# Kernel tuning notes

Measured on AMD Instinct MI355X. Metric: run time of the kernel, lower is better.

## Reference

```python
import jax, jax.numpy as jnp
import numpy as np

N_QUBITS = 12
N_LAYERS = 3


def _apply_ry(state, theta, q):
    # state: (2,)*n real statevector; RY on qubit q
    c = jnp.cos(theta * 0.5)
    s = jnp.sin(theta * 0.5)
    st = jnp.moveaxis(state, q, 0)
    st = jnp.stack([c * st[0] - s * st[1], s * st[0] + c * st[1]])
    return jnp.moveaxis(st, 0, q)


def _apply_cz(state, q, r):
    st = jnp.moveaxis(state, (q, r), (0, 1))
    st = st.at[1, 1].multiply(-1.0)
    return jnp.moveaxis(st, (0, 1), (q, r))


def _embed(x, params):
    # angle-embedding ansatz: L layers of RY(theta[l,q]+x[q]) + CZ ring
    n = N_QUBITS
    state = jnp.zeros((2,) * n, dtype=x.dtype).at[(0,) * n].set(1.0)
    for l in range(N_LAYERS):
        for q in range(n):
            state = _apply_ry(state, params[l, q] + x[q], q)
        for q in range(n):
            state = _apply_cz(state, q, (q + 1) % n)
    return state.reshape(-1)  # (2^n,)


def setup_inputs() -> dict:
    key = jax.random.key(0)
    k1, k2, k3 = jax.random.split(key, 3)
    data = jax.random.uniform(k1, (2048, N_QUBITS), dtype=jnp.float32)
    labels = jax.random.randint(k2, (2048,), 0, 2, dtype=jnp.int32)
    params = jax.random.normal(k3, (N_LAYERS, N_QUBITS), dtype=jnp.float32)
    return {"data": data, "labels": labels, "params": params}


def reference(data, labels, params):
    # Psi[i] = U(x_i, params)|0>, k_ij = |<psi_j|psi_i>|^2 (== prob of amp 0 of U^dag(x_j)U(x_i)|0>)
    psi = jax.vmap(_embed, in_axes=(0, None))(data, params)  # (N, 2^n)
    K = jnp.square(psi @ psi.T)                              # (N, N) pairwise kernel
    lab = 2.0 * labels.astype(psi.dtype) - 1.0               # {0,1} -> {-1,+1}
    LL = jnp.outer(lab, lab)
    kernel_polarity = jnp.sum(LL * K)
    square_sum_k = jnp.sum(K * K)
    square_sum_l = jnp.sum(LL * LL)
    return kernel_polarity / jnp.sqrt(square_sum_k * square_sum_l)
```

## Files before the change

kernel.cpp:

```cpp
#include <hip/hip_runtime.h>
#include <math.h>

#define NQ    12
#define DIM   4096
#define K_EXT 4096
#define KSL   512
#define NSAMP 2048
#define NLAY  3
#define NT2   16
#define NTRI2 136
#define NSLICE 8
#define BK    64

typedef __attribute__((ext_vector_type(8)))  short bf16x8;
typedef __attribute__((ext_vector_type(16))) float floatx16;

__device__ __forceinline__ unsigned short f32_to_bf16(float x) {
    unsigned u = __builtin_bit_cast(unsigned, x);
    u += 0x7FFFu + ((u >> 16) & 1u);
    return (unsigned short)(u >> 16);
}

__device__ __forceinline__ void gl_lds16(const unsigned short* g, unsigned short* l) {
    __builtin_amdgcn_global_load_lds(
        (const __attribute__((address_space(1))) unsigned int*)g,
        (__attribute__((address_space(3))) unsigned int*)l,
        16, 0, 0);
}

__device__ __forceinline__ void tri_decode(int bid, int& bi, int& bj) {
    int i = (int)((33.0 - sqrt(33.0*33.0 - 8.0*(double)bid)) * 0.5);
    int start = i*(33-i)/2;
    while (bid < start)               { --i; start = i*(33-i)/2; }
    while (bid >= start + (NT2 - i))  { start += NT2 - i; ++i; }
    bi = i; bj = i + (bid - start);
}

__global__ __launch_bounds__(256) void sim_kernel(const float* __restrict__ data,
                                                  const float* __restrict__ params,
                                                  unsigned short* __restrict__ pe,
                                                  double* __restrict__ acc,
                                                  unsigned* __restrict__ cnt)
{
    __shared__ float CS[2*36], SN[2*36];
    __shared__ float trans[2][4608];
    const int tid  = threadIdx.x;
    const int wave = tid >> 6, lane = tid & 63;
    const int sidx = wave >> 1;
    const int w    = wave & 1;
    const int smp  = blockIdx.x * 2 + sidx;

    if (blockIdx.x == 0 && tid == 0) {
        acc[0] = 0.0; acc[1] = 0.0; cnt[0] = 0u;
    }

    if (w == 0 && lane < NLAY*NQ) {
        const int q = lane % NQ;
        const float th = 0.5f * (params[lane] + data[smp*NQ + q]);
        CS[sidx*36 + lane] = cosf(th);
        SN[sidx*36 + lane] = sinf(th);
    }
    __syncthreads();

    float v[32];

    float* buf = trans[sidx];
    float* wb  = buf + 36*lane + 2304*w;
    const float* rb = buf + ((lane>>2)&15) + 16*w + 36*(lane&3);

    {
        const float* cs = &CS[sidx*36];
        const float* sn = &SN[sidx*36];
        const int hi = (lane >> 2) & 15;
        float fx = ((lane & 1) ? sn[0] : cs[0]) * ((lane & 2) ? sn[1] : cs[1]);
        fx *= ((hi & 1) ? sn[7]  : cs[7]);
        fx *= ((hi & 2) ? sn[8]  : cs[8]);
        fx *= ((hi & 4) ? sn[9]  : cs[9]);
        fx *= ((hi & 8) ? sn[10] : cs[10]);
        fx *= (w ? sn[11] : cs[11]);
        v[0] = fx * cs[2];
        v[1] = fx * sn[2];
        #pragma unroll
        for (int b = 1; b < 5; ++b) {
            const int M = 1 << b;
            #pragma unroll
            for (int r = 0; r < 32; ++r) {
                if (r < M) {
                    v[r | M] = v[r] * sn[2 + b];
                    v[r]     = v[r] * cs[2 + b];
                }
            }
        }
        const int Base = (lane & 3) | (hi << 7) | (w << 11);
        #pragma unroll
        for (int r = 0; r < 32; ++r) {
            const int i  = Base | (r << 2);
            const int t  = ((i >> 1) | (i << 11)) & 0xFFF;
            const int p  = __popc(i & t) & 1;
            v[r] = __builtin_bit_cast(float, __builtin_bit_cast(int, v[r]) ^ (p << 31));
        }
    }

    #pragma unroll 1
    for (int l = 1; l < NLAY; ++l) {
        const float* cs = &CS[sidx*36 + l*NQ];
        const float* sn = &SN[sidx*36 + l*NQ];
        const int even = !(l & 1);

        {
            const int qb = even ? 7 : 2;
            #pragma unroll
            for (int b = 0; b < 5; ++b) {
                const float c = cs[qb + b], s = sn[qb + b];
                const int M = 1 << b;
                #pragma unroll
                for (int r = 0; r < 32; ++r) {
                    if (!(r & M)) {
                        const float a0 = v[r], a1 = v[r | M];
                        v[r]     = c * a0 - s * a1;
                        v[r | M] = s * a0 + c * a1;
                    }
                }
            }
        }
        {
            const float c0 = cs[0], s0 = sn[0];
            const float t0 = (lane & 1) ? s0 : -s0;
            #pragma unroll
            for (int r = 0; r < 32; ++r) {
                const int iv = __builtin_bit_cast(int, v[r]);
                const int pv = __builtin_amdgcn_update_dpp(0, iv, 0xB1, 0xF, 0xF, true);
                v[r] = c0 * v[r] + t0 * __builtin_bit_cast(float, pv);
            }
            const float c1 = cs[1], s1 = sn[1];
            const float t1 = (lane & 2) ? s1 : -s1;
            #pragma unroll
            for (int r = 0; r < 32; ++r) {
                const int iv = __builtin_bit_cast(int, v[r]);
                const int pv = __builtin_amdgcn_update_dpp(0, iv, 0x4E, 0xF, 0xF, true);
                v[r] = c1 * v[r] + t1 * __builtin_bit_cast(float, pv);
            }
        }
        __syncthreads();
        #pragma unroll
        for (int t = 0; t < 8; ++t) {
            float4 q4;
            q4.x = v[4*t]; q4.y = v[4*t+1]; q4.z = v[4*t+2]; q4.w = v[4*t+3];
            *(float4*)&wb[4*t] = q4;
        }
        __syncthreads();
        #pragma unroll
        for (int r = 0; r < 32; ++r)
            v[r] = rb[144*(r & 15) + 2304*(r >> 4)];

        {
            const int qb = even ? 2 : 7;
            #pragma unroll
            for (int b = 0; b < 5; ++b) {
                const float c = cs[qb + b], s = sn[qb + b];
                const int M = 1 << b;
                #pragma unroll
                for (int r = 0; r < 32; ++r) {
                    if (!(r & M)) {
                        const float a0 = v[r], a1 = v[r | M];
                        v[r]     = c * a0 - s * a1;
                        v[r | M] = s * a0 + c * a1;
                    }
                }
            }
        }
        {
            const int Base = even ? ((lane & 3) | (((lane >> 2) & 15) << 7) | (w << 11))
                                  : (lane | (w << 6));
            const int shift = even ? 2 : 7;
            #pragma unroll
            for (int r = 0; r < 32; ++r) {
                const int i  = Base | (r << shift);
                const int t  = ((i >> 1) | (i << 11)) & 0xFFF;
                const int p  = __popc(i & t) & 1;
                v[r] = __builtin_bit_cast(float, __builtin_bit_cast(int, v[r]) ^ (p << 31));
            }
        }
    }

    const int sw = smp & 7;
    const int ell = w*64 + lane;
    unsigned short* outb = pe + (size_t)smp * K_EXT;
    #pragma unroll
    for (int c = 0; c < 4; ++c) {
        uint4 H;
        H.x = (unsigned)f32_to_bf16(v[c*8+0]) | ((unsigned)f32_to_bf16(v[c*8+1]) << 16);
        H.y = (unsigned)f32_to_bf16(v[c*8+2]) | ((unsigned)f32_to_bf16(v[c*8+3]) << 16);
        H.z = (unsigned)f32_to_bf16(v[c*8+4]) | ((unsigned)f32_to_bf16(v[c*8+5]) << 16);
        H.w = (unsigned)f32_to_bf16(v[c*8+6]) | ((unsigned)f32_to_bf16(v[c*8+7]) << 16);
        const int gc  = 4*ell + c;
        const int pos = (gc & ~7) | ((gc ^ sw) & 7);
        *(uint4*)&outb[pos*8] = H;
    }
}

__global__ __launch_bounds__(256) void gram_partial(const unsigned short* __restrict__ pe,
                                                    float* __restrict__ Gp)
{
    __shared__ __align__(16) unsigned short stage[2][2*128*64];

    const int tid   = threadIdx.x;
    const int tile  = blockIdx.x >> 3;
    const int slice = blockIdx.x & 7;
    int bi, bj; tri_decode(tile, bi, bj);
    const int k0 = slice * KSL;

    const int wave = tid >> 6, lane = tid & 63;
    const int qr = (wave >> 1) * 64;
    const int qc = (wave &  1) * 64;
    const int mrow = lane & 31;
    const int chsel = lane >> 5;
    const int sw = mrow & 7;

    floatx16 c00, c01, c10, c11;
    #pragma unroll
    for (int i = 0; i < 16; ++i) { c00[i]=0.f; c01[i]=0.f; c10[i]=0.f; c11[i]=0.f; }

    const int mat  = wave >> 1;
    const int half = wave & 1;
    const unsigned short* gbase = pe
        + ((size_t)((mat ? bj : bi)*128 + half*64 + (lane >> 3))) * K_EXT
        + k0 + (lane & 7)*8;
    const int lofs = mat*128*64 + half*64*64;

    {
        unsigned short* l = &stage[0][lofs];
        #pragma unroll
        for (int i = 0; i < 8; ++i)
            gl_lds16(gbase + (size_t)i*8*K_EXT, l + i*512);
    }
    __syncthreads();

    int cur = 0;
    #pragma unroll 1
    for (int kk = 0; kk < KSL; kk += BK) {
        if (kk + BK < KSL) {
            unsigned short* l = &stage[cur ^ 1][lofs];
            const unsigned short* g = gbase + kk + BK;
            #pragma unroll
            for (int i = 0; i < 8; ++i)
                gl_lds16(g + (size_t)i*8*K_EXT, l + i*512);
        }

        const unsigned short* As = &stage[cur][0];
        const unsigned short* Bs = &stage[cur][128*64];
        #pragma unroll
        for (int ks = 0; ks < 4; ++ks) {
            const int ch = (ks*2 + chsel) ^ sw;
            const bf16x8 a0 = *(const bf16x8*)&As[(qr +      mrow)*64 + ch*8];
            const bf16x8 a1 = *(const bf16x8*)&As[(qr + 32 + mrow)*64 + ch*8];
            const bf16x8 b0 = *(const bf16x8*)&Bs[(qc +      mrow)*64 + ch*8];
            const bf16x8 b1 = *(const bf16x8*)&Bs[(qc + 32 + mrow)*64 + ch*8];
            c00 = __builtin_amdgcn_mfma_f32_32x32x16_bf16(a0, b0, c00, 0, 0, 0);
            c01 = __builtin_amdgcn_mfma_f32_32x32x16_bf16(a0, b1, c01, 0, 0, 0);
            c10 = __builtin_amdgcn_mfma_f32_32x32x16_bf16(a1, b0, c10, 0, 0, 0);
            c11 = __builtin_amdgcn_mfma_f32_32x32x16_bf16(a1, b1, c11, 0, 0, 0);
        }
        __syncthreads();
        cur ^= 1;
    }

    float* Gt = Gp + ((size_t)slice * NTRI2 + tile) * 16384;
    const int crow = chsel * 4;
    const int ccol = lane & 31;
    #pragma unroll
    for (int rr = 0; rr < 16; ++rr) {
        const int rl = (rr & 3) + 8*(rr >> 2) + crow;
        const int r0 = qr + rl,  r1 = qr + 32 + rl;
        const int cA = qc + ccol, cB = qc + 32 + ccol;
        Gt[r0*128 + cA] = c00[rr];
        Gt[r0*128 + cB] = c01[rr];
        Gt[r1*128 + cA] = c10[rr];
        Gt[r1*128 + cB] = c11[rr];
    }
}

__global__ __launch_bounds__(256) void gram_reduce(const float* __restrict__ Gp,
                                                   const int* __restrict__ labels,
                                                   double* __restrict__ acc,
                                                   unsigned* __restrict__ cnt,
                                                   float* __restrict__ out)
{
    __shared__ float la[128], lb[128];
    __shared__ double red1[256], red2[256];
    const int tid  = threadIdx.x;
    const int tile = blockIdx.x >> 2;
    const int quar = blockIdx.x & 3;
    int bi, bj; tri_decode(tile, bi, bj);

    if (tid < 128) la[tid]       = 2.0f*(float)labels[bi*128 + tid]       - 1.0f;
    else           lb[tid - 128] = 2.0f*(float)labels[bj*128 + tid - 128] - 1.0f;
    __syncthreads();

    const size_t stride = (size_t)NTRI2 * 16384;
    const float* g0 = Gp + (size_t)tile * 16384 + quar * 4096;

    double s1 = 0.0, s2 = 0.0;
    #pragma unroll
    for (int u = 0; u < 4; ++u) {
        const int e = u*1024 + tid*4;
        float4 g = make_float4(0.f, 0.f, 0.f, 0.f);
        #pragma unroll
        for (int s = 0; s < NSLICE; ++s) {
            const float4 t = *(const float4*)&g0[e + (size_t)s*stride];
            g.x += t.x; g.y += t.y; g.z += t.z; g.w += t.w;
        }
        const int ge  = quar*4096 + e;
        const int row = ge >> 7, c0 = ge & 127;
        const float lr = la[row];
        const float gg[4] = {g.x, g.y, g.z, g.w};
        #pragma unroll
        for (int j = 0; j < 4; ++j) {
            const int col = c0 + j;
            const float w = (bi < bj) ? 2.0f : ((row < col) ? 2.0f : ((row == col) ? 1.0f : 0.0f));
            const float g2 = gg[j] * gg[j];
            s1 += (double)(w * lr * lb[col] * g2);
            const double d = (double)g2;
            s2 += (double)w * d * d;
        }
    }

    red1[tid] = s1; red2[tid] = s2; __syncthreads();
    for (int off = 128; off; off >>= 1) {
        if (tid < off) { red1[tid] += red1[tid+off]; red2[tid] += red2[tid+off]; }
        __syncthreads();
    }
    if (tid == 0) {
        atomicAdd(&acc[0], red1[0]);
        atomicAdd(&acc[1], red2[0]);
        __threadfence();
        const unsigned old = atomicAdd(cnt, 1u);
        if (old == NTRI2*4 - 1) {
            const double t1 = atomicAdd(&acc[0], 0.0);
            const double t2 = atomicAdd(&acc[1], 0.0);
            out[0] = (float)(t1 / (sqrt(t2) * (double)NSAMP));
        }
    }
}

extern "C" void kernel_launch(void* const* d_in, const int* in_sizes, int n_in,
                              void* d_out, int out_size, void* d_ws, size_t ws_size,
                              hipStream_t stream)
{
    const float* data   = (const float*)d_in[0];
    const int*   labels = (const int*)d_in[1];
    const float* params = (const float*)d_in[2];

    double*   acc = (double*)d_ws;
    unsigned* cnt = (unsigned*)((char*)d_ws + 64);
    unsigned short* psi = (unsigned short*)((char*)d_ws + 16384);
    float* Gp = (float*)((char*)d_ws + 16384 + (size_t)NSAMP*K_EXT*2);

    sim_kernel<<<NSAMP/2, 256, 0, stream>>>(data, params, psi, acc, cnt);
    gram_partial<<<NTRI2*NSLICE, 256, 0, stream>>>(psi, Gp);
    gram_reduce<<<NTRI2*4, 256, 0, stream>>>(Gp, labels, acc, cnt, (float*)d_out);
}
```

Measured before the change: 138.3 us.

## Fuse gram reduction into split-K kernel via per-tile completion counters

Removes the separate reduce kernel: each gram_partial block bumps a per-tile counter, and the last slice block for a tile sums the partials and accumulates the polarity terms. The split-K factor is halved, giving longer K per block and fewer partial buffers to write and read. This saves a launch and some partial-sum traffic. In exchange the reduction runs on only one block per tile with scalar atomic loads, and there are fewer blocks to fill the GPU.

```diff
diff --git a/kernel.cpp b/kernel.cpp
--- a/kernel.cpp
+++ b/kernel.cpp
@@ -4,12 +4,12 @@
 #define NQ    12
 #define DIM   4096
 #define K_EXT 4096
-#define KSL   512
+#define KSL   1024
 #define NSAMP 2048
 #define NLAY  3
 #define NT2   16
 #define NTRI2 136
-#define NSLICE 8
+#define NSLICE 4
 #define BK    64
 
 typedef __attribute__((ext_vector_type(8)))  short bf16x8;
@@ -40,7 +40,8 @@
                                                   const float* __restrict__ params,
                                                   unsigned short* __restrict__ pe,
                                                   double* __restrict__ acc,
-                                                  unsigned* __restrict__ cnt)
+                                                  unsigned* __restrict__ gcnt,
+                                                  unsigned* __restrict__ tcnt)
 {
     __shared__ float CS[2*36], SN[2*36];
     __shared__ float trans[2][4608];
@@ -50,8 +51,9 @@
     const int w    = wave & 1;
     const int smp  = blockIdx.x * 2 + sidx;
 
-    if (blockIdx.x == 0 && tid == 0) {
-        acc[0] = 0.0; acc[1] = 0.0; cnt[0] = 0u;
+    if (blockIdx.x == 0) {
+        if (tid == 0) { acc[0] = 0.0; acc[1] = 0.0; gcnt[0] = 0u; }
+        if (tid < NTRI2) tcnt[tid] = 0u;
     }
 
     if (w == 0 && lane < NLAY*NQ) {
@@ -200,13 +202,19 @@
 }
 
 __global__ __launch_bounds__(256) void gram_partial(const unsigned short* __restrict__ pe,
-                                                    float* __restrict__ Gp)
+                                                    float* __restrict__ Gp,
+                                                    const int* __restrict__ labels,
+                                                    double* __restrict__ acc,
+                                                    unsigned* __restrict__ gcnt,
+                                                    unsigned* __restrict__ tcnt,
+                                                    float* __restrict__ out)
 {
     __shared__ __align__(16) unsigned short stage[2][2*128*64];
+    __shared__ unsigned sord;
 
     const int tid   = threadIdx.x;
-    const int tile  = blockIdx.x >> 3;
-    const int slice = blockIdx.x & 7;
+    const int tile  = blockIdx.x >> 2;
+    const int slice = blockIdx.x & 3;
     int bi, bj; tri_decode(tile, bi, bj);
     const int k0 = slice * KSL;
 
@@ -278,51 +286,37 @@
         Gt[r1*128 + cA] = c10[rr];
         Gt[r1*128 + cB] = c11[rr];
     }
-}
-
-__global__ __launch_bounds__(256) void gram_reduce(const float* __restrict__ Gp,
-                                                   const int* __restrict__ labels,
-                                                   double* __restrict__ acc,
-                                                   unsigned* __restrict__ cnt,
-                                                   float* __restrict__ out)
-{
-    __shared__ float la[128], lb[128];
-    __shared__ double red1[256], red2[256];
-    const int tid  = threadIdx.x;
-    const int tile = blockIdx.x >> 2;
-    const int quar = blockIdx.x & 3;
-    int bi, bj; tri_decode(tile, bi, bj);
-
+
+    __threadfence();
+    if (tid == 0) sord = atomicAdd(&tcnt[tile], 1u);
+    __syncthreads();
+    if (sord != NSLICE - 1) return;
+
+    float*  la   = (float*)&stage[0][0];
+    float*  lb   = la + 128;
+    double* red1 = (double*)(la + 256);
+    double* red2 = red1 + 256;
     if (tid < 128) la[tid]       = 2.0f*(float)labels[bi*128 + tid]       - 1.0f;
     else           lb[tid - 128] = 2.0f*(float)labels[bj*128 + tid - 128] - 1.0f;
     __syncthreads();
 
     const size_t stride = (size_t)NTRI2 * 16384;
-    const float* g0 = Gp + (size_t)tile * 16384 + quar * 4096;
-
+    const float* g0 = Gp + (size_t)tile * 16384;
     double s1 = 0.0, s2 = 0.0;
-    #pragma unroll
-    for (int u = 0; u < 4; ++u) {
-        const int e = u*1024 + tid*4;
-        float4 g = make_float4(0.f, 0.f, 0.f, 0.f);
-        #pragma unroll
-        for (int s = 0; s < NSLICE; ++s) {
-            const float4 t = *(const float4*)&g0[e + (size_t)s*stride];
-            g.x += t.x; g.y += t.y; g.z += t.z; g.w += t.w;
-        }
-        const int ge  = quar*4096 + e;
-        const int row = ge >> 7, c0 = ge & 127;
-        const float lr = la[row];
-        const float gg[4] = {g.x, g.y, g.z, g.w};
-        #pragma unroll
-        for (int j = 0; j < 4; ++j) {
-            const int col = c0 + j;
-            const float w = (bi < bj) ? 2.0f : ((row < col) ? 2.0f : ((row == col) ? 1.0f : 0.0f));
-            const float g2 = gg[j] * gg[j];
-            s1 += (double)(w * lr * lb[col] * g2);
-            const double d = (double)g2;
-            s2 += (double)w * d * d;
-        }
+    #pragma unroll 2
+    for (int u = 0; u < 64; ++u) {
+        const int e = u*256 + tid;
+        float g = 0.f;
+        #pragma unroll
+        for (int s = 0; s < NSLICE; ++s)
+            g += __hip_atomic_load(&g0[e + (size_t)s*stride],
+                                   __ATOMIC_RELAXED, __HIP_MEMORY_SCOPE_AGENT);
+        const int row = e >> 7, col = e & 127;
+        const float w = (bi < bj) ? 2.0f : ((row < col) ? 2.0f : ((row == col) ? 1.0f : 0.0f));
+        const float g2 = g * g;
+        s1 += (double)(w * la[row] * lb[col] * g2);
+        const double d = (double)g2;
+        s2 += (double)w * d * d;
     }
 
     red1[tid] = s1; red2[tid] = s2; __syncthreads();
@@ -334,8 +328,8 @@
         atomicAdd(&acc[0], red1[0]);
         atomicAdd(&acc[1], red2[0]);
         __threadfence();
-        const unsigned old = atomicAdd(cnt, 1u);
-        if (old == NTRI2*4 - 1) {
+        const unsigned old = atomicAdd(gcnt, 1u);
+        if (old == NTRI2 - 1) {
             const double t1 = atomicAdd(&acc[0], 0.0);
             const double t2 = atomicAdd(&acc[1], 0.0);
             out[0] = (float)(t1 / (sqrt(t2) * (double)NSAMP));
@@ -351,12 +345,13 @@
     const int*   labels = (const int*)d_in[1];
     const float* params = (const float*)d_in[2];
 
-    double*   acc = (double*)d_ws;
-    unsigned* cnt = (unsigned*)((char*)d_ws + 64);
+    double*   acc  = (double*)d_ws;
+    unsigned* gcnt = (unsigned*)((char*)d_ws + 64);
+    unsigned* tcnt = (unsigned*)((char*)d_ws + 128);
     unsigned short* psi = (unsigned short*)((char*)d_ws + 16384);
     float* Gp = (float*)((char*)d_ws + 16384 + (size_t)NSAMP*K_EXT*2);
 
-    sim_kernel<<<NSAMP/2, 256, 0, stream>>>(data, params, psi, acc, cnt);
-    gram_partial<<<NTRI2*NSLICE, 256, 0, stream>>>(psi, Gp);
-    gram_reduce<<<NTRI2*4, 256, 0, stream>>>(Gp, labels, acc, cnt, (float*)d_out);
-}
+    sim_kernel<<<NSAMP/2, 256, 0, stream>>>(data, params, psi, acc, gcnt, tcnt);
+    gram_partial<<<NTRI2*NSLICE, 256, 0, stream>>>(psi, Gp, labels, acc, gcnt, tcnt,
+                                                   (float*)d_out);
+}
```

Result: slower. 205.8 us (+48.9%).
